# Kernel tuning notes

Measured on AMD Instinct MI355X. Metric: run time of the kernel, lower is better.

Reference implementation:

```python
import jax, jax.numpy as jnp
import numpy as np

B, DIM, N, K, NA = 1, 64, 1024, 16, 12
POS_HID = 64
ATTN_HID = 4 * DIM


def setup_inputs() -> dict:
    key = jax.random.key(0)
    ks = jax.random.split(key, 8)
    s = 0.05  # small init scale, mimics xavier magnitude
    return {
        "xyz": jax.random.normal(ks[0], (B, 3, N), jnp.float32),
        "feats": jax.random.normal(ks[1], (B, DIM, N, NA), jnp.float32),
        "anchors": jax.random.normal(ks[2], (NA, 3, 3), jnp.float32),
        "to_qkv": jax.random.normal(ks[3], (3 * DIM, DIM), jnp.float32) * s,
        "pos_mlp1": jax.random.normal(ks[4], (POS_HID, 3), jnp.float32) * s,
        "pos_mlp2": jax.random.normal(ks[5], (DIM, POS_HID), jnp.float32) * s,
        "attn_mlp1": jax.random.normal(ks[6], (ATTN_HID, DIM), jnp.float32) * s,
        "attn_mlp2": jax.random.normal(ks[7], (DIM, ATTN_HID), jnp.float32) * s,
    }


def reference(xyz, feats, anchors, to_qkv, pos_mlp1, pos_mlp2, attn_mlp1, attn_mlp2):
    # --- KNN over points (self included) ---
    pts = jnp.swapaxes(xyz, 1, 2)                      # [B,N,3]
    sq = jnp.sum(pts * pts, axis=-1)                   # [B,N]
    d2 = sq[:, :, None] + sq[:, None, :] - 2.0 * jnp.einsum('bnd,bmd->bnm', pts, pts)
    _, idx = jax.lax.top_k(-d2, K)                     # [B,N,K] nearest indices

    # --- gather helpers (vmapped over batch) ---
    gather3 = jax.vmap(lambda x, i: x[:, i])           # [C,N],[N,K] -> [C,N,K]
    gather4 = jax.vmap(lambda x, i: x[:, i, :])        # [C,N,A],[N,K] -> [C,N,K,A]

    # --- relative positions rotated by anchors ---
    grouped_xyz = gather3(xyz, idx)                    # [B,3,N,K]
    rel = xyz[:, :, :, None] - grouped_xyz             # [B,3,N,K]
    gx = jnp.einsum('aij,bjnk->binka', anchors, rel)   # [B,3,N,K,NA]

    # --- positional embedding MLP ---
    pe = jnp.einsum('ji,binka->bjnka', pos_mlp1, gx)   # [B,POS_HID,N,K,NA]
    pe = jax.nn.relu(pe)
    pe = jnp.einsum('ji,binka->bjnka', pos_mlp2, pe)   # [B,DIM,N,K,NA]

    # --- qkv projection ---
    qkv = jnp.einsum('ji,bina->bjna', to_qkv, feats)   # [B,3*DIM,N,NA]
    q, k, v = jnp.split(qkv, 3, axis=1)                # each [B,DIM,N,NA]

    k_g = gather4(k, idx)                              # [B,DIM,N,K,NA]
    v_g = gather4(v, idx) + pe                         # [B,DIM,N,K,NA]
    qk_rel = q[:, :, :, None, :] - k_g                 # [B,DIM,N,K,NA]

    # --- attention MLP on (qk_rel + pe) ---
    sim = qk_rel + pe
    sim = jnp.einsum('ji,binka->bjnka', attn_mlp1, sim)  # [B,4*DIM,N,K,NA]
    sim = jax.nn.relu(sim)
    sim = jnp.einsum('ji,binka->bjnka', attn_mlp2, sim)  # [B,DIM,N,K,NA]

    # --- per-channel softmax over neighbor axis, aggregate ---
    attn = jax.nn.softmax(sim, axis=-2)
    return jnp.sum(attn * v_g, axis=-2)                # [B,DIM,N,NA]
```

## Files before the change

kernel.cpp:

```cpp
#include <hip/hip_runtime.h>

#define NPTS 1024
#define DIM 64
#define KNN 16
#define NA 12
#define NCOL 192
#define XPAD 68

typedef __attribute__((ext_vector_type(8))) short bf16x8;
typedef __attribute__((ext_vector_type(4))) float f32x4;

static __device__ inline unsigned short f2bfu(float x) {
    __bf16 b = (__bf16)x;
    return __builtin_bit_cast(unsigned short, b);
}
static __device__ inline bf16x8 load8_cvt(const float* p) {
    f32x4 u = *(const f32x4*)p;
    f32x4 v = *(const f32x4*)(p + 4);
    bf16x8 r;
    r[0] = (short)f2bfu(u[0]); r[1] = (short)f2bfu(u[1]); r[2] = (short)f2bfu(u[2]); r[3] = (short)f2bfu(u[3]);
    r[4] = (short)f2bfu(v[0]); r[5] = (short)f2bfu(v[1]); r[6] = (short)f2bfu(v[2]); r[7] = (short)f2bfu(v[3]);
    return r;
}

__global__ __launch_bounds__(256) void prep_kernel(const float* __restrict__ feats,
                                                   const float* __restrict__ to_qkv,
                                                   float* __restrict__ qkvT,
                                                   unsigned short* __restrict__ pack,
                                                   const float* __restrict__ pos2,
                                                   const float* __restrict__ am1,
                                                   const float* __restrict__ am2,
                                                   const float* __restrict__ xyz,
                                                   int* __restrict__ idxout) {
    __shared__ unsigned short XT[16][72];
    __shared__ float px[NPTS], py[NPTS], pz[NPTS];
    const int b = blockIdx.x;
    const int t = threadIdx.x;
    const int n0 = b * 16;
    const bool do_knn = (b < 256);

    if (b < 72 && t < 64) {
        int s = b;
        int c16p = t & 15, gp = t >> 4;
        const float* src;
        if (s < 8) {
            int nt = s >> 1, kt = s & 1;
            src = pos2 + (nt * 16 + c16p) * 64 + kt * 32 + gp * 8;
        } else if (s < 40) {
            int u = s - 8, hq = u >> 3, nt = (u >> 1) & 3, kt = u & 1;
            src = am1 + (hq * 64 + nt * 16 + c16p) * 64 + kt * 32 + gp * 8;
        } else {
            int u = s - 40, hq = u >> 3, nt = (u >> 1) & 3, kt = u & 1;
            src = am2 + (nt * 16 + c16p) * 256 + hq * 64 + kt * 32 + gp * 8;
        }
        unsigned short* dst = pack + (s * 64 + t) * 8;
        #pragma unroll
        for (int e = 0; e < 8; ++e) dst[e] = f2bfu(src[e]);
    }

    if (do_knn) {
        for (int m = t; m < NPTS; m += 256) {
            px[m] = xyz[m];
            py[m] = xyz[NPTS + m];
            pz[m] = xyz[2 * NPTS + m];
        }
    }
    for (int e = t; e < 16 * 64; e += 256) {
        int c = e & 15, i = e >> 4;
        XT[c][i] = f2bfu(feats[i * (NPTS * NA) + n0 + c]);
    }
    __syncthreads();

    const int lane = t & 63, w = t >> 6, c16 = lane & 15, g = lane >> 4;

    {
        const f32x4 zero4 = {0.f, 0.f, 0.f, 0.f};
        f32x4 acc[3] = {zero4, zero4, zero4};
        #pragma unroll
        for (int kt = 0; kt < 2; ++kt) {
            bf16x8 af = *(const bf16x8*)&XT[c16][kt * 32 + g * 8];
            #pragma unroll
            for (int ni = 0; ni < 3; ++ni) {
                int cd = (w * 3 + ni) * 16 + c16;
                bf16x8 bfr = load8_cvt(to_qkv + cd * 64 + kt * 32 + g * 8);
                acc[ni] = __builtin_amdgcn_mfma_f32_16x16x32_bf16(af, bfr, acc[ni], 0, 0, 0);
            }
        }
        #pragma unroll
        for (int ni = 0; ni < 3; ++ni) {
            int cd = (w * 3 + ni) * 16 + c16;
            int c = cd >> 6, d = cd & 63;
            #pragma unroll
            for (int r = 0; r < 4; ++r) {
                int na = n0 + 4 * g + r;
                qkvT[c * (NPTS * NA * DIM) + na * 64 + d] = acc[ni][r];
            }
        }
    }

    if (do_knn) {
        const int n = b * 4 + w;
        const float xn = px[n], yn = py[n], zn = pz[n];
        const float sqn = xn * xn + yn * yn + zn * zn;
        float dd[16]; int id[16];
        #pragma unroll
        for (int j = 0; j < 16; ++j) {
            int m = j * 64 + lane;
            float xm = px[m], ym = py[m], zm = pz[m];
            float sqm = xm * xm + ym * ym + zm * zm;
            float dot = xn * xm + yn * ym + zn * zm;
            dd[j] = sqn + sqm - 2.f * dot;
            id[j] = m;
        }
        for (int r = 0; r < KNN; ++r) {
            float bd = 1e30f; int bi = 0x7fffffff;
            #pragma unroll
            for (int j = 0; j < 16; ++j)
                if (dd[j] < bd || (dd[j] == bd && id[j] < bi)) { bd = dd[j]; bi = id[j]; }
            #pragma unroll
            for (int mask = 1; mask < 64; mask <<= 1) {
                float od = __shfl_xor(bd, mask);
                int oi = __shfl_xor(bi, mask);
                if (od < bd || (od == bd && oi < bi)) { bd = od; bi = oi; }
            }
            if (lane == 0) idxout[n * KNN + r] = bi;
            #pragma unroll
            for (int j = 0; j < 16; ++j)
                if (id[j] == bi) dd[j] = 1e30f;
        }
    }
}

__global__ __launch_bounds__(512, 4) void attn_main(const float* __restrict__ xyz,
                                                    const float* __restrict__ anchors,
                                                    const float* __restrict__ pos1,
                                                    const unsigned short* __restrict__ pack,
                                                    const float* __restrict__ qT,
                                                    const float* __restrict__ kT,
                                                    const float* __restrict__ vT,
                                                    const int* __restrict__ nn,
                                                    float* __restrict__ out) {
    __shared__ __align__(16) unsigned short XbT[NCOL][XPAD];
    __shared__ __align__(16) unsigned short HqT[NCOL][XPAD];

    int*   nidx = (int*)&HqT[0][0];
    float* relb = (float*)nidx + 16;
    float* ab   = relb + 48;
    float* gbuf = ab + 108;

    const int n = blockIdx.x, t = threadIdx.x;
    const int lane = t & 63, wave = t >> 6;
    const int c16 = lane & 15, g = lane >> 4;
    const int mw = wave & 3;
    const int nw = wave >> 2;

    if (t < 108) ab[t] = anchors[t];
    if (t < KNN) {
        int m = nn[n * KNN + t];
        nidx[t] = m;
        relb[t * 3 + 0] = xyz[n] - xyz[m];
        relb[t * 3 + 1] = xyz[NPTS + n] - xyz[NPTS + m];
        relb[t * 3 + 2] = xyz[2 * NPTS + n] - xyz[2 * NPTS + m];
    }
    __syncthreads();

    for (int e = t; e < 3 * NCOL; e += 512) {
        int row = e / NCOL, col = e % NCOL;
        int a = col >> 4, k = col & 15;
        gbuf[row * NCOL + col] = ab[a * 9 + row * 3 + 0] * relb[k * 3 + 0]
                               + ab[a * 9 + row * 3 + 1] * relb[k * 3 + 1]
                               + ab[a * 9 + row * 3 + 2] * relb[k * 3 + 2];
    }
    __syncthreads();

    {
        const float p10 = pos1[lane * 3 + 0], p11 = pos1[lane * 3 + 1], p12 = pos1[lane * 3 + 2];
        #pragma unroll
        for (int j = 0; j < 24; ++j) {
            int col = wave + 8 * j;
            float p = p10 * gbuf[col] + p11 * gbuf[NCOL + col] + p12 * gbuf[2 * NCOL + col];
            XbT[col][lane] = f2bfu(p > 0.f ? p : 0.f);
        }
    }
    __syncthreads();

    const bf16x8* pk16 = (const bf16x8*)pack;
    const f32x4 zero4 = {0.f, 0.f, 0.f, 0.f};

    f32x4 peacc[6] = {zero4, zero4, zero4, zero4, zero4, zero4};
    #pragma unroll
    for (int kt = 0; kt < 2; ++kt) {
        bf16x8 b0 = pk16[((2 * nw + 0) * 2 + kt) * 64 + lane];
        bf16x8 b1 = pk16[((2 * nw + 1) * 2 + kt) * 64 + lane];
        #pragma unroll
        for (int mi = 0; mi < 3; ++mi) {
            bf16x8 af = *(const bf16x8*)&XbT[(mw + 4 * mi) * 16 + c16][kt * 32 + g * 8];
            peacc[mi * 2 + 0] = __builtin_amdgcn_mfma_f32_16x16x32_bf16(af, b0, peacc[mi * 2 + 0], 0, 0, 0);
            peacc[mi * 2 + 1] = __builtin_amdgcn_mfma_f32_16x16x32_bf16(af, b1, peacc[mi * 2 + 1], 0, 0, 0);
        }
    }

    float vgk[6][4], xreg[6][4];
    {
        const int m0 = nidx[4 * g + 0], m1 = nidx[4 * g + 1];
        const int m2 = nidx[4 * g + 2], m3 = nidx[4 * g + 3];
        #pragma unroll
        for (int mi = 0; mi < 3; ++mi) {
            int a = mw + 4 * mi;
            #pragma unroll
            for (int ni = 0; ni < 2; ++ni) {
                int tile = mi * 2 + ni;
                int d = (2 * nw + ni) * 16 + c16;
                float qv = qT[(n * NA + a) * DIM + d];
                int b0 = (m0 * NA + a) * DIM + d, b1 = (m1 * NA + a) * DIM + d;
                int b2 = (m2 * NA + a) * DIM + d, b3 = (m3 * NA + a) * DIM + d;
                xreg[tile][0] = qv - kT[b0] + peacc[tile][0]; vgk[tile][0] = vT[b0] + peacc[tile][0];
                xreg[tile][1] = qv - kT[b1] + peacc[tile][1]; vgk[tile][1] = vT[b1] + peacc[tile][1];
                xreg[tile][2] = qv - kT[b2] + peacc[tile][2]; vgk[tile][2] = vT[b2] + peacc[tile][2];
                xreg[tile][3] = qv - kT[b3] + peacc[tile][3]; vgk[tile][3] = vT[b3] + peacc[tile][3];
            }
        }
    }
    __syncthreads();
    #pragma unroll
    for (int mi = 0; mi < 3; ++mi)
        #pragma unroll
        for (int ni = 0; ni < 2; ++ni) {
            int tile = mi * 2 + ni;
            int col = (2 * nw + ni) * 16 + c16;
            #pragma unroll
            for (int r = 0; r < 4; ++r)
                XbT[(mw + 4 * mi) * 16 + 4 * g + r][col] = f2bfu(xreg[tile][r]);
        }
    __syncthreads();

    f32x4 sacc[6] = {zero4, zero4, zero4, zero4, zero4, zero4};
    for (int hq = 0; hq < 4; ++hq) {
        f32x4 hacc[6] = {zero4, zero4, zero4, zero4, zero4, zero4};
        #pragma unroll
        for (int kt = 0; kt < 2; ++kt) {
            bf16x8 b0 = pk16[(8 + (hq * 4 + 2 * nw + 0) * 2 + kt) * 64 + lane];
            bf16x8 b1 = pk16[(8 + (hq * 4 + 2 * nw + 1) * 2 + kt) * 64 + lane];
            #pragma unroll
            for (int mi = 0; mi < 3; ++mi) {
                bf16x8 af = *(const bf16x8*)&XbT[(mw + 4 * mi) * 16 + c16][kt * 32 + g * 8];
                hacc[mi * 2 + 0] = __builtin_amdgcn_mfma_f32_16x16x32_bf16(af, b0, hacc[mi * 2 + 0], 0, 0, 0);
                hacc[mi * 2 + 1] = __builtin_amdgcn_mfma_f32_16x16x32_bf16(af, b1, hacc[mi * 2 + 1], 0, 0, 0);
            }
        }
        #pragma unroll
        for (int mi = 0; mi < 3; ++mi)
            #pragma unroll
            for (int ni = 0; ni < 2; ++ni) {
                int tile = mi * 2 + ni;
                int col = (2 * nw + ni) * 16 + c16;
                #pragma unroll
                for (int r = 0; r < 4; ++r)
                    HqT[(mw + 4 * mi) * 16 + 4 * g + r][col] = f2bfu(fmaxf(hacc[tile][r], 0.f));
            }
        __syncthreads();
        #pragma unroll
        for (int kt = 0; kt < 2; ++kt) {
            bf16x8 b0 = pk16[(40 + hq * 8 + (2 * nw + 0) * 2 + kt) * 64 + lane];
            bf16x8 b1 = pk16[(40 + hq * 8 + (2 * nw + 1) * 2 + kt) * 64 + lane];
            #pragma unroll
            for (int mi = 0; mi < 3; ++mi) {
                bf16x8 af = *(const bf16x8*)&HqT[(mw + 4 * mi) * 16 + c16][kt * 32 + g * 8];
                sacc[mi * 2 + 0] = __builtin_amdgcn_mfma_f32_16x16x32_bf16(af, b0, sacc[mi * 2 + 0], 0, 0, 0);
                sacc[mi * 2 + 1] = __builtin_amdgcn_mfma_f32_16x16x32_bf16(af, b1, sacc[mi * 2 + 1], 0, 0, 0);
            }
        }
        __syncthreads();
    }

    #pragma unroll
    for (int mi = 0; mi < 3; ++mi) {
        int a = mw + 4 * mi;
        #pragma unroll
        for (int ni = 0; ni < 2; ++ni) {
            int tile = mi * 2 + ni;
            int d = (2 * nw + ni) * 16 + c16;
            float e0 = __expf(sacc[tile][0]);
            float e1 = __expf(sacc[tile][1]);
            float e2 = __expf(sacc[tile][2]);
            float e3 = __expf(sacc[tile][3]);
            float den = (e0 + e1) + (e2 + e3);
            float num = (e0 * vgk[tile][0] + e1 * vgk[tile][1]) + (e2 * vgk[tile][2] + e3 * vgk[tile][3]);
            den += __shfl_xor(den, 16); num += __shfl_xor(num, 16);
            den += __shfl_xor(den, 32); num += __shfl_xor(num, 32);
            if (g == 0)
                out[(d * NPTS + n) * NA + a] = num / den;
        }
    }
}

extern "C" void kernel_launch(void* const* d_in, const int* in_sizes, int n_in,
                              void* d_out, int out_size, void* d_ws, size_t ws_size,
                              hipStream_t stream) {
    const float* xyz     = (const float*)d_in[0];
    const float* feats   = (const float*)d_in[1];
    const float* anchors = (const float*)d_in[2];
    const float* to_qkv  = (const float*)d_in[3];
    const float* pos1    = (const float*)d_in[4];
    const float* pos2    = (const float*)d_in[5];
    const float* am1     = (const float*)d_in[6];
    const float* am2     = (const float*)d_in[7];
    float* out = (float*)d_out;

    float* ws = (float*)d_ws;
    const int seg = NPTS * NA * DIM;
    float* qT = ws;
    float* kT = ws + seg;
    float* vT = ws + 2 * seg;
    int* nn = (int*)(ws + 3 * seg);
    unsigned short* pack = (unsigned short*)(ws + 3 * seg + NPTS * KNN);

    prep_kernel<<<768, 256, 0, stream>>>(feats, to_qkv, qT, pack, pos2, am1, am2, xyz, nn);
    attn_main<<<NPTS, 512, 0, stream>>>(xyz, anchors, pos1, pack, qT, kT, vT, nn, out);
}
```

Before: 79.94 us.

## Double-buffer hidden-layer LDS tile and drop per-iteration barriers

Adds a second shared-memory buffer for the attention MLP hidden chunk and alternates between the two across hq iterations, so the trailing __syncthreads in each iteration can be removed. The positional hidden activations now go into one of the H buffers, which lets the q-k+pe values be written straight into XbT without a separate register staging pass and its extra barrier. The aim is fewer block-wide barriers and less register pressure. The cost is about 26 KB more LDS per block, which may reduce how many blocks fit on a CU.

```diff
diff --git a/kernel.cpp b/kernel.cpp
--- a/kernel.cpp
+++ b/kernel.cpp
@@ -141,9 +141,10 @@
                                                     const int* __restrict__ nn,
                                                     float* __restrict__ out) {
     __shared__ __align__(16) unsigned short XbT[NCOL][XPAD];
-    __shared__ __align__(16) unsigned short HqT[NCOL][XPAD];
-
-    int*   nidx = (int*)&HqT[0][0];
+    __shared__ __align__(16) unsigned short Hq0[NCOL][XPAD];
+    __shared__ __align__(16) unsigned short Hq1[NCOL][XPAD];
+
+    int*   nidx = (int*)&Hq0[0][0];
     float* relb = (float*)nidx + 16;
     float* ab   = relb + 48;
     float* gbuf = ab + 108;
@@ -179,7 +180,7 @@
         for (int j = 0; j < 24; ++j) {
             int col = wave + 8 * j;
             float p = p10 * gbuf[col] + p11 * gbuf[NCOL + col] + p12 * gbuf[2 * NCOL + col];
-            XbT[col][lane] = f2bfu(p > 0.f ? p : 0.f);
+            Hq1[col][lane] = f2bfu(p > 0.f ? p : 0.f);
         }
     }
     __syncthreads();
@@ -194,13 +195,13 @@
         bf16x8 b1 = pk16[((2 * nw + 1) * 2 + kt) * 64 + lane];
         #pragma unroll
         for (int mi = 0; mi < 3; ++mi) {
-            bf16x8 af = *(const bf16x8*)&XbT[(mw + 4 * mi) * 16 + c16][kt * 32 + g * 8];
+            bf16x8 af = *(const bf16x8*)&Hq1[(mw + 4 * mi) * 16 + c16][kt * 32 + g * 8];
             peacc[mi * 2 + 0] = __builtin_amdgcn_mfma_f32_16x16x32_bf16(af, b0, peacc[mi * 2 + 0], 0, 0, 0);
             peacc[mi * 2 + 1] = __builtin_amdgcn_mfma_f32_16x16x32_bf16(af, b1, peacc[mi * 2 + 1], 0, 0, 0);
         }
     }
 
-    float vgk[6][4], xreg[6][4];
+    float vgk[6][4];
     {
         const int m0 = nidx[4 * g + 0], m1 = nidx[4 * g + 1];
         const int m2 = nidx[4 * g + 2], m3 = nidx[4 * g + 3];
@@ -211,31 +212,27 @@
             for (int ni = 0; ni < 2; ++ni) {
                 int tile = mi * 2 + ni;
                 int d = (2 * nw + ni) * 16 + c16;
+                int col = (2 * nw + ni) * 16 + c16;
                 float qv = qT[(n * NA + a) * DIM + d];
                 int b0 = (m0 * NA + a) * DIM + d, b1 = (m1 * NA + a) * DIM + d;
                 int b2 = (m2 * NA + a) * DIM + d, b3 = (m3 * NA + a) * DIM + d;
-                xreg[tile][0] = qv - kT[b0] + peacc[tile][0]; vgk[tile][0] = vT[b0] + peacc[tile][0];
-                xreg[tile][1] = qv - kT[b1] + peacc[tile][1]; vgk[tile][1] = vT[b1] + peacc[tile][1];
-                xreg[tile][2] = qv - kT[b2] + peacc[tile][2]; vgk[tile][2] = vT[b2] + peacc[tile][2];
-                xreg[tile][3] = qv - kT[b3] + peacc[tile][3]; vgk[tile][3] = vT[b3] + peacc[tile][3];
-            }
-        }
-    }
-    __syncthreads();
+                float x0 = qv - kT[b0] + peacc[tile][0]; vgk[tile][0] = vT[b0] + peacc[tile][0];
+                float x1 = qv - kT[b1] + peacc[tile][1]; vgk[tile][1] = vT[b1] + peacc[tile][1];
+                float x2 = qv - kT[b2] + peacc[tile][2]; vgk[tile][2] = vT[b2] + peacc[tile][2];
+                float x3 = qv - kT[b3] + peacc[tile][3]; vgk[tile][3] = vT[b3] + peacc[tile][3];
+                XbT[(mw + 4 * mi) * 16 + 4 * g + 0][col] = f2bfu(x0);
+                XbT[(mw + 4 * mi) * 16 + 4 * g + 1][col] = f2bfu(x1);
+                XbT[(mw + 4 * mi) * 16 + 4 * g + 2][col] = f2bfu(x2);
+                XbT[(mw + 4 * mi) * 16 + 4 * g + 3][col] = f2bfu(x3);
+            }
+        }
+    }
+    __syncthreads();
+
+    f32x4 sacc[6] = {zero4, zero4, zero4, zero4, zero4, zero4};
     #pragma unroll
-    for (int mi = 0; mi < 3; ++mi)
-        #pragma unroll
-        for (int ni = 0; ni < 2; ++ni) {
-            int tile = mi * 2 + ni;
-            int col = (2 * nw + ni) * 16 + c16;
-            #pragma unroll
-            for (int r = 0; r < 4; ++r)
-                XbT[(mw + 4 * mi) * 16 + 4 * g + r][col] = f2bfu(xreg[tile][r]);
-        }
-    __syncthreads();
-
-    f32x4 sacc[6] = {zero4, zero4, zero4, zero4, zero4, zero4};
     for (int hq = 0; hq < 4; ++hq) {
+        unsigned short (*Hc)[XPAD] = (hq & 1) ? Hq1 : Hq0;
         f32x4 hacc[6] = {zero4, zero4, zero4, zero4, zero4, zero4};
         #pragma unroll
         for (int kt = 0; kt < 2; ++kt) {
@@ -256,7 +253,7 @@
                 int col = (2 * nw + ni) * 16 + c16;
                 #pragma unroll
                 for (int r = 0; r < 4; ++r)
-                    HqT[(mw + 4 * mi) * 16 + 4 * g + r][col] = f2bfu(fmaxf(hacc[tile][r], 0.f));
+                    Hc[(mw + 4 * mi) * 16 + 4 * g + r][col] = f2bfu(fmaxf(hacc[tile][r], 0.f));
             }
         __syncthreads();
         #pragma unroll
@@ -265,12 +262,11 @@
             bf16x8 b1 = pk16[(40 + hq * 8 + (2 * nw + 1) * 2 + kt) * 64 + lane];
             #pragma unroll
             for (int mi = 0; mi < 3; ++mi) {
-                bf16x8 af = *(const bf16x8*)&HqT[(mw + 4 * mi) * 16 + c16][kt * 32 + g * 8];
+                bf16x8 af = *(const bf16x8*)&Hc[(mw + 4 * mi) * 16 + c16][kt * 32 + g * 8];
                 sacc[mi * 2 + 0] = __builtin_amdgcn_mfma_f32_16x16x32_bf16(af, b0, sacc[mi * 2 + 0], 0, 0, 0);
                 sacc[mi * 2 + 1] = __builtin_amdgcn_mfma_f32_16x16x32_bf16(af, b1, sacc[mi * 2 + 1], 0, 0, 0);
             }
         }
-        __syncthreads();
     }
 
     #pragma unroll
```

Result: slower. 95.36 us (+19.3%).
